# Kernel optimization log

Measured on AMD Instinct MI355X. Metric: run time of the kernel, lower is better.

Reference implementation:

```python
import jax, jax.numpy as jnp
import numpy as np

B, C, E, H = 8, 2048, 1024, 128


def setup_inputs() -> dict:
    key = jax.random.key(0)
    kx, kq, kk, kv = jax.random.split(key, 4)
    scale = 1.0 / np.sqrt(E)
    return {
        "x": jax.random.normal(kx, (B, C, E), dtype=jnp.float32),
        "Wq": jax.random.normal(kq, (E, H), dtype=jnp.float32) * scale,
        "Wk": jax.random.normal(kk, (E, H), dtype=jnp.float32) * scale,
        "Wv": jax.random.normal(kv, (E, H), dtype=jnp.float32) * scale,
    }


def reference(x, Wq, Wk, Wv):
    # x: (B, C, E); projections -> (B, C, H)
    q = jnp.einsum("bce,eh->bch", x, Wq)
    k = jnp.einsum("bce,eh->bch", x, Wk)
    v = jnp.einsum("bce,eh->bch", x, Wv)
    # NOTE: original scales by sqrt(embed_size), not head_size
    scores = jnp.einsum("bqh,bkh->bqk", q, k) / jnp.sqrt(jnp.asarray(E, x.dtype))
    Cq = x.shape[1]
    causal = jnp.tril(jnp.ones((Cq, Cq), dtype=bool))
    scores = jnp.where(causal, scores, -jnp.inf)
    weights = jax.nn.softmax(scores, axis=-1)  # (B, C, C)
    out = jnp.einsum("bqk,bkh->bqh", weights, v)
    return out
```

## Files before the change

kernel.cpp:

```cpp
#include <hip/hip_runtime.h>
#include <hip/hip_bf16.h>

#define BATCH 8
#define CTX   2048
#define EMB   1024
#define HD    128
#define VSTR  2080

using bf16x8 = __attribute__((ext_vector_type(8))) short;
using fx4    = __attribute__((ext_vector_type(4))) float;

__device__ __forceinline__ ushort f2bf(float f) {
    union { float f; unsigned u; } v; v.f = f;
    unsigned u = v.u;
    u += 0x7fffu + ((u >> 16) & 1u);
    return (ushort)(u >> 16);
}

__device__ __forceinline__ unsigned cvtpk(float a, float b) {
    unsigned r;
    asm("v_cvt_pk_bf16_f32 %0, %1, %2" : "=v"(r) : "v"(a), "v"(b));
    return r;
}

__device__ __forceinline__ void gload16(const void* g, void* l) {
    __builtin_amdgcn_global_load_lds(
        (const __attribute__((address_space(1))) unsigned*)g,
        (__attribute__((address_space(3))) unsigned*)l, 16, 0, 0);
}

__global__ void wt_kernel(const float* __restrict__ Wq, const float* __restrict__ Wk,
                          const float* __restrict__ Wv, ushort* __restrict__ Wt) {
    int idx = blockIdx.x * blockDim.x + threadIdx.x;
    int e = idx % EMB;
    int h = (idx / EMB) % HD;
    int w = idx / (EMB * HD);
    const float* W = (w == 0) ? Wq : (w == 1) ? Wk : Wv;
    Wt[idx] = f2bf(W[e * HD + h]);
}

__global__ __launch_bounds__(256) void proj_kernel(
        const float* __restrict__ x, const ushort* __restrict__ Wt,
        ushort* __restrict__ q, ushort* __restrict__ k, ushort* __restrict__ vt) {
    __shared__ __align__(16) char As[2][4096];
    __shared__ __align__(16) char Bs[2][24576];

    const int t    = threadIdx.x;
    const int wave = t >> 6;
    const int lane = t & 63;
    const int lo = lane & 15, hi = lane >> 4;
    const int brow = blockIdx.x * 32;

    fx4 acc[2][6];
#pragma unroll
    for (int m2 = 0; m2 < 2; m2++)
#pragma unroll
        for (int n = 0; n < 6; n++) acc[m2][n] = fx4{0.f, 0.f, 0.f, 0.f};

    const int arow  = t >> 3;
    const int aslot = (t & 7) ^ (arow & 7);
    const float* asrc = x + (size_t)(brow + arow) * EMB + aslot * 4;

    const ushort* bsrc[6];
#pragma unroll
    for (int r = 0; r < 6; r++) {
        const int lrow = r * 32 + (t >> 3);
        const int u    = (t & 7) ^ (lrow & 7);
        bsrc[r] = Wt + (size_t)(lrow * 2 + (u >> 2)) * EMB + (u & 3) * 8;
    }

#define PSTAGE(bi, k0_) do {                                          \
    gload16(asrc + (k0_), As[bi] + wave * 1024);                      \
    _Pragma("unroll")                                                 \
    for (int r = 0; r < 6; ++r)                                       \
        gload16(bsrc[r] + (k0_), Bs[bi] + r * 4096 + wave * 1024);    \
} while (0)

    PSTAGE(0, 0);
    for (int it = 0; it < 32; ++it) {
        if (it + 1 < 32) {
            PSTAGE((it + 1) & 1, (it + 1) * 32);
            asm volatile("s_waitcnt vmcnt(7)" ::: "memory");
        } else {
            asm volatile("s_waitcnt vmcnt(0)" ::: "memory");
        }
        __builtin_amdgcn_sched_barrier(0);
        __builtin_amdgcn_s_barrier();
        __builtin_amdgcn_sched_barrier(0);

        const char* Ab = As[it & 1];
        const char* Bb = Bs[it & 1];

        bf16x8 af[2];
#pragma unroll
        for (int m2 = 0; m2 < 2; m2++) {
            const int rowA = m2 * 16 + lo;
            const int s0 = (hi * 2) ^ (rowA & 7);
            const int s1 = (hi * 2 + 1) ^ (rowA & 7);
            fx4 a0 = *(const fx4*)(Ab + rowA * 128 + s0 * 16);
            fx4 a1 = *(const fx4*)(Ab + rowA * 128 + s1 * 16);
            union { unsigned u[4]; bf16x8 v; } pk;
            pk.u[0] = cvtpk(a0[0], a0[1]);
            pk.u[1] = cvtpk(a0[2], a0[3]);
            pk.u[2] = cvtpk(a1[0], a1[1]);
            pk.u[3] = cvtpk(a1[2], a1[3]);
            af[m2] = pk.v;
        }
        __builtin_amdgcn_s_setprio(1);
#pragma unroll
        for (int n = 0; n < 6; n++) {
            const int col  = wave * 96 + n * 16 + lo;
            const int rowp = col >> 1;
            const int slot = ((col & 1) * 4 + hi) ^ (rowp & 7);
            bf16x8 bfr = *(const bf16x8*)(Bb + rowp * 128 + slot * 16);
#pragma unroll
            for (int m2 = 0; m2 < 2; m2++)
                acc[m2][n] = __builtin_amdgcn_mfma_f32_16x16x32_bf16(af[m2], bfr, acc[m2][n], 0, 0, 0);
        }
        __builtin_amdgcn_s_setprio(0);
        __builtin_amdgcn_s_barrier();
    }
#undef PSTAGE

    const float qscale = 0.03125f;
#pragma unroll
    for (int n = 0; n < 6; n++) {
        const int col = wave * 96 + n * 16 + lo;
        const int bnn = col >> 7;
        const int cc  = col & 127;
#pragma unroll
        for (int m2 = 0; m2 < 2; m2++) {
#pragma unroll
            for (int j = 0; j < 4; j++) {
                const int r = brow + m2 * 16 + hi * 4 + j;
                if (bnn == 0)      q[(size_t)r * HD + cc] = f2bf(acc[m2][n][j] * qscale);
                else if (bnn == 1) k[(size_t)r * HD + cc] = f2bf(acc[m2][n][j]);
                else {
                    const int bb = r >> 11, ccc = r & (CTX - 1);
                    vt[((size_t)bb * HD + cc) * VSTR + ccc] = f2bf(acc[m2][n][j]);
                }
            }
        }
    }
}

__global__ __launch_bounds__(128) void attn_kernel(
        const ushort* __restrict__ q, const ushort* __restrict__ k,
        const ushort* __restrict__ vt, float* __restrict__ out) {
    __shared__ __align__(16) char Ks[2][16384];
    __shared__ __align__(16) char Vs[2][16384];
    __shared__ __align__(16) char p_lds[2][1024];

    const int id   = blockIdx.x;
    const int b    = id & 7;
    const int pos  = id >> 3;
    const int qt   = 127 - pos;
    const int q0   = qt * 16;
    const int t    = threadIdx.x;
    const int w    = t >> 6;
    const int lane = t & 63;
    const int lo = lane & 15, hi = lane >> 4;

    const ushort* qb = q  + (size_t)b * CTX * HD;
    const ushort* kb = k  + (size_t)b * CTX * HD;
    const ushort* vb = vt + (size_t)b * HD * VSTR;

    bf16x8 qf[4];
#pragma unroll
    for (int ks = 0; ks < 4; ks++)
        qf[ks] = *(const bf16x8*)(qb + (q0 + lo) * HD + ks * 32 + hi * 8);

    fx4 o[8];
#pragma unroll
    for (int h = 0; h < 8; h++) o[h] = fx4{0.f, 0.f, 0.f, 0.f};
    float m[4], l[4];
#pragma unroll
    for (int j = 0; j < 4; j++) { m[j] = 0.f; l[j] = 0.f; }

    const int krow = t >> 4;
    const int ksl  = ((t & 15) ^ (krow & 7)) << 3;
    const int vrow = t >> 3;
    const int vsl  = ((t & 7) ^ (vrow & 7)) << 3;

#define STAGE(bi, kv0_) do {                                          \
    _Pragma("unroll")                                                 \
    for (int r = 0; r < 8; ++r)                                       \
        gload16(kb + (size_t)((kv0_) + r * 8 + krow) * HD + ksl,      \
                Ks[bi] + r * 2048 + w * 1024);                        \
    _Pragma("unroll")                                                 \
    for (int r = 0; r < 8; ++r)                                       \
        gload16(vb + (size_t)(r * 16 + vrow) * VSTR + (kv0_) + vsl,   \
                Vs[bi] + r * 2048 + w * 1024);                        \
} while (0)

    const int nkv = qt / 4 + 1;
    STAGE(0, 0);
    for (int it = 0; it < nkv; ++it) {
        if (it + 1 < nkv) {
            STAGE((it + 1) & 1, (it + 1) * 64);
            asm volatile("s_waitcnt vmcnt(16)" ::: "memory");
        } else {
            asm volatile("s_waitcnt vmcnt(0)" ::: "memory");
        }
        __builtin_amdgcn_sched_barrier(0);
        __builtin_amdgcn_s_barrier();
        __builtin_amdgcn_sched_barrier(0);

        const char* Kb = Ks[it & 1];
        const char* Vb = Vs[it & 1];
        const int kv0 = it * 64;

        fx4 s[2];
        s[0] = fx4{0.f, 0.f, 0.f, 0.f};
        s[1] = fx4{0.f, 0.f, 0.f, 0.f};
        __builtin_amdgcn_s_setprio(1);
#pragma unroll
        for (int n2 = 0; n2 < 2; n2++) {
            const int row = w * 32 + n2 * 16 + lo;
            const unsigned sw = (unsigned)((row & 7) << 4);
#pragma unroll
            for (int ks = 0; ks < 4; ks++) {
                bf16x8 kf = *(const bf16x8*)(Kb + row * 256 + ((ks * 64 + hi * 16) ^ sw));
                s[n2] = __builtin_amdgcn_mfma_f32_16x16x32_bf16(qf[ks], kf, s[n2], 0, 0, 0);
            }
        }
        __builtin_amdgcn_s_setprio(0);

        const bool diag = (kv0 + 64 > q0);
        float pmax[4];
        int allok = 1;
#pragma unroll
        for (int j = 0; j < 4; j++) {
            const int r = q0 + hi * 4 + j;
            if (diag) {
#pragma unroll
                for (int n2 = 0; n2 < 2; n2++)
                    if ((kv0 + w * 32 + n2 * 16 + lo) > r) s[n2][j] = -INFINITY;
            }
            pmax[j] = fmaxf(s[0][j], s[1][j]);
            allok &= (pmax[j] <= m[j] + 16.0f);
        }
        if (!__all(allok)) {
#pragma unroll
            for (int j = 0; j < 4; j++) {
                float mx = pmax[j];
                mx = fmaxf(mx, __shfl_xor(mx, 1));
                mx = fmaxf(mx, __shfl_xor(mx, 2));
                mx = fmaxf(mx, __shfl_xor(mx, 4));
                mx = fmaxf(mx, __shfl_xor(mx, 8));
                const float mn = fmaxf(m[j], mx);
                const float f  = __expf(m[j] - mn);
                l[j] *= f;
#pragma unroll
                for (int h = 0; h < 8; h++) o[h][j] *= f;
                m[j] = mn;
            }
        }
#pragma unroll
        for (int j = 0; j < 4; j++) {
            float sum = 0.f;
#pragma unroll
            for (int n2 = 0; n2 < 2; n2++) {
                const float pv = __expf(s[n2][j] - m[j]);
                s[n2][j] = pv;
                sum += pv;
            }
            l[j] += sum;
            const int row = hi * 4 + j;
            const unsigned sw = (unsigned)((row & 3) << 4);
#pragma unroll
            for (int n2 = 0; n2 < 2; n2++) {
                const unsigned cb = (unsigned)((n2 * 16 + lo) * 2);
                *(ushort*)(p_lds[w] + row * 64 + (cb ^ sw)) = f2bf(s[n2][j]);
            }
        }
        asm volatile("" ::: "memory");
        bf16x8 pa = *(const bf16x8*)(p_lds[w] + lo * 64 + ((hi * 16) ^ ((lo & 3) << 4)));
        __builtin_amdgcn_s_setprio(1);
#pragma unroll
        for (int h = 0; h < 8; h++) {
            const int vr = h * 16 + lo;
            bf16x8 vf = *(const bf16x8*)(Vb + vr * 128 + ((w * 64 + hi * 16) ^ ((vr & 7) << 4)));
            o[h] = __builtin_amdgcn_mfma_f32_16x16x32_bf16(pa, vf, o[h], 0, 0, 0);
        }
        __builtin_amdgcn_s_setprio(0);
        __builtin_amdgcn_s_barrier();
    }
#undef STAGE

#pragma unroll
    for (int j = 0; j < 4; j++) {
        l[j] += __shfl_xor(l[j], 1);
        l[j] += __shfl_xor(l[j], 2);
        l[j] += __shfl_xor(l[j], 4);
        l[j] += __shfl_xor(l[j], 8);
    }

    float* oB  = (float*)Ks[0];
    float* mlB = (float*)Vs[0];
    __syncthreads();
    if (w == 1) {
#pragma unroll
        for (int j = 0; j < 4; j++) {
            const int row = hi * 4 + j;
            if (lo == 0) { mlB[row] = m[j]; mlB[16 + row] = l[j]; }
#pragma unroll
            for (int h = 0; h < 8; h++) oB[row * 128 + h * 16 + lo] = o[h][j];
        }
    }
    __syncthreads();
    if (w == 0) {
        float* ob = out + ((size_t)b * CTX + q0) * HD;
#pragma unroll
        for (int j = 0; j < 4; j++) {
            const int row = hi * 4 + j;
            const float mB = mlB[row], lB = mlB[16 + row];
            const float mt = fmaxf(m[j], mB);
            const float fA = __expf(m[j] - mt);
            const float fB = __expf(mB - mt);
            const float inv = 1.0f / (l[j] * fA + lB * fB);
#pragma unroll
            for (int h = 0; h < 8; h++)
                ob[row * HD + h * 16 + lo] =
                    (o[h][j] * fA + oB[row * 128 + h * 16 + lo] * fB) * inv;
        }
    }
}

extern "C" void kernel_launch(void* const* d_in, const int* in_sizes, int n_in,
                              void* d_out, int out_size, void* d_ws, size_t ws_size,
                              hipStream_t stream) {
    const float* x  = (const float*)d_in[0];
    const float* Wq = (const float*)d_in[1];
    const float* Wk = (const float*)d_in[2];
    const float* Wv = (const float*)d_in[3];

    ushort* Wt = (ushort*)d_ws;
    ushort* qw = (ushort*)((char*)d_ws + 786432);
    ushort* kw = qw + (size_t)BATCH * CTX * HD;
    ushort* vw = kw + (size_t)BATCH * CTX * HD;

    wt_kernel<<<(3 * HD * EMB) / 256, 256, 0, stream>>>(Wq, Wk, Wv, Wt);
    proj_kernel<<<(BATCH * CTX) / 32, 256, 0, stream>>>(x, Wt, qw, kw, vw);
    attn_kernel<<<1024, 128, 0, stream>>>(qw, kw, vw, (float*)d_out);
}
```

Measured before the change: 100.6 us.

## Share KV tiles across two query tiles per block and restructure projection pipeline

The attention kernel now runs 256 threads per block covering 32 query rows (two 16-row halves), so each staged K/V tile in LDS is reused by twice as many queries. The grid is halved and the causal tile order is reordered for load balance. The loop now issues the next stage after a full wait plus barrier, which removes the trailing barrier. The projection kernel triple-buffers the x tile and issues the next prefetch after the barrier, also dropping the trailing barrier. The trade-off is more LDS and registers per block and possibly less overlap between loads and compute in attention, since the wait is now vmcnt(0).

```diff
diff --git a/kernel.cpp b/kernel.cpp
--- a/kernel.cpp
+++ b/kernel.cpp
@@ -42,7 +42,7 @@
 __global__ __launch_bounds__(256) void proj_kernel(
         const float* __restrict__ x, const ushort* __restrict__ Wt,
         ushort* __restrict__ q, ushort* __restrict__ k, ushort* __restrict__ vt) {
-    __shared__ __align__(16) char As[2][4096];
+    __shared__ __align__(16) char As[3][4096];
     __shared__ __align__(16) char Bs[2][24576];
 
     const int t    = threadIdx.x;
@@ -69,26 +69,28 @@
         bsrc[r] = Wt + (size_t)(lrow * 2 + (u >> 2)) * EMB + (u & 3) * 8;
     }
 
-#define PSTAGE(bi, k0_) do {                                          \
-    gload16(asrc + (k0_), As[bi] + wave * 1024);                      \
-    _Pragma("unroll")                                                 \
-    for (int r = 0; r < 6; ++r)                                       \
-        gload16(bsrc[r] + (k0_), Bs[bi] + r * 4096 + wave * 1024);    \
-} while (0)
-
-    PSTAGE(0, 0);
+    gload16(asrc + 0, As[0] + wave * 1024);
+#pragma unroll
+    for (int r = 0; r < 6; ++r)
+        gload16(bsrc[r] + 0, Bs[0] + r * 4096 + wave * 1024);
+    gload16(asrc + 32, As[1] + wave * 1024);
+
     for (int it = 0; it < 32; ++it) {
-        if (it + 1 < 32) {
-            PSTAGE((it + 1) & 1, (it + 1) * 32);
-            asm volatile("s_waitcnt vmcnt(7)" ::: "memory");
-        } else {
-            asm volatile("s_waitcnt vmcnt(0)" ::: "memory");
-        }
+        if (it == 31) asm volatile("s_waitcnt vmcnt(0)" ::: "memory");
+        else          asm volatile("s_waitcnt vmcnt(1)" ::: "memory");
         __builtin_amdgcn_sched_barrier(0);
         __builtin_amdgcn_s_barrier();
         __builtin_amdgcn_sched_barrier(0);
 
-        const char* Ab = As[it & 1];
+        if (it + 1 < 32) {
+#pragma unroll
+            for (int r = 0; r < 6; ++r)
+                gload16(bsrc[r] + (it + 1) * 32, Bs[(it + 1) & 1] + r * 4096 + wave * 1024);
+            if (it + 2 < 32)
+                gload16(asrc + (it + 2) * 32, As[(it + 2) % 3] + wave * 1024);
+        }
+
+        const char* Ab = As[it % 3];
         const char* Bb = Bs[it & 1];
 
         bf16x8 af[2];
@@ -118,9 +120,7 @@
                 acc[m2][n] = __builtin_amdgcn_mfma_f32_16x16x32_bf16(af[m2], bfr, acc[m2][n], 0, 0, 0);
         }
         __builtin_amdgcn_s_setprio(0);
-        __builtin_amdgcn_s_barrier();
-    }
-#undef PSTAGE
+    }
 
     const float qscale = 0.03125f;
 #pragma unroll
@@ -144,22 +144,23 @@
     }
 }
 
-__global__ __launch_bounds__(128) void attn_kernel(
+__global__ __launch_bounds__(256) void attn_kernel(
         const ushort* __restrict__ q, const ushort* __restrict__ k,
         const ushort* __restrict__ vt, float* __restrict__ out) {
     __shared__ __align__(16) char Ks[2][16384];
     __shared__ __align__(16) char Vs[2][16384];
-    __shared__ __align__(16) char p_lds[2][1024];
+    __shared__ __align__(16) char p_lds[4][1024];
 
     const int id   = blockIdx.x;
     const int b    = id & 7;
     const int pos  = id >> 3;
-    const int qt   = 127 - pos;
-    const int q0   = qt * 16;
+    const int qt   = (pos < 32) ? (63 - pos) : (pos - 32);
     const int t    = threadIdx.x;
-    const int w    = t >> 6;
+    const int wave = t >> 6;
     const int lane = t & 63;
     const int lo = lane & 15, hi = lane >> 4;
+    const int wq = wave & 1, w = wave >> 1;
+    const int q0 = qt * 32 + wq * 16;
 
     const ushort* qb = q  + (size_t)b * CTX * HD;
     const ushort* kb = k  + (size_t)b * CTX * HD;
@@ -177,34 +178,29 @@
 #pragma unroll
     for (int j = 0; j < 4; j++) { m[j] = 0.f; l[j] = 0.f; }
 
-    const int krow = t >> 4;
-    const int ksl  = ((t & 15) ^ (krow & 7)) << 3;
-    const int vrow = t >> 3;
-    const int vsl  = ((t & 7) ^ (vrow & 7)) << 3;
-
-#define STAGE(bi, kv0_) do {                                          \
-    _Pragma("unroll")                                                 \
-    for (int r = 0; r < 8; ++r)                                       \
-        gload16(kb + (size_t)((kv0_) + r * 8 + krow) * HD + ksl,      \
-                Ks[bi] + r * 2048 + w * 1024);                        \
-    _Pragma("unroll")                                                 \
-    for (int r = 0; r < 8; ++r)                                       \
-        gload16(vb + (size_t)(r * 16 + vrow) * VSTR + (kv0_) + vsl,   \
-                Vs[bi] + r * 2048 + w * 1024);                        \
+#define STAGE(bi, kv0_) do {                                                   \
+    _Pragma("unroll")                                                          \
+    for (int r = 0; r < 4; ++r) {                                              \
+        const int row = r * 16 + (t >> 4);                                     \
+        gload16(kb + (size_t)((kv0_) + row) * HD + (((t & 15) ^ (row & 7)) << 3), \
+                Ks[bi] + r * 4096 + wave * 1024);                              \
+    }                                                                          \
+    _Pragma("unroll")                                                          \
+    for (int r = 0; r < 4; ++r) {                                              \
+        const int row = r * 32 + (t >> 3);                                     \
+        gload16(vb + (size_t)row * VSTR + (kv0_) + (((t & 7) ^ (row & 7)) << 3), \
+                Vs[bi] + r * 4096 + wave * 1024);                              \
+    }                                                                          \
 } while (0)
 
-    const int nkv = qt / 4 + 1;
+    const int nkv = qt / 2 + 1;
     STAGE(0, 0);
     for (int it = 0; it < nkv; ++it) {
-        if (it + 1 < nkv) {
-            STAGE((it + 1) & 1, (it + 1) * 64);
-            asm volatile("s_waitcnt vmcnt(16)" ::: "memory");
-        } else {
-            asm volatile("s_waitcnt vmcnt(0)" ::: "memory");
-        }
+        asm volatile("s_waitcnt vmcnt(0)" ::: "memory");
         __builtin_amdgcn_sched_barrier(0);
         __builtin_amdgcn_s_barrier();
         __builtin_amdgcn_sched_barrier(0);
+        if (it + 1 < nkv) STAGE((it + 1) & 1, (it + 1) * 64);
 
         const char* Kb = Ks[it & 1];
         const char* Vb = Vs[it & 1];
@@ -271,11 +267,11 @@
 #pragma unroll
             for (int n2 = 0; n2 < 2; n2++) {
                 const unsigned cb = (unsigned)((n2 * 16 + lo) * 2);
-                *(ushort*)(p_lds[w] + row * 64 + (cb ^ sw)) = f2bf(s[n2][j]);
+                *(ushort*)(p_lds[wave] + row * 64 + (cb ^ sw)) = f2bf(s[n2][j]);
             }
         }
         asm volatile("" ::: "memory");
-        bf16x8 pa = *(const bf16x8*)(p_lds[w] + lo * 64 + ((hi * 16) ^ ((lo & 3) << 4)));
+        bf16x8 pa = *(const bf16x8*)(p_lds[wave] + lo * 64 + ((hi * 16) ^ ((lo & 3) << 4)));
         __builtin_amdgcn_s_setprio(1);
 #pragma unroll
         for (int h = 0; h < 8; h++) {
@@ -284,7 +280,6 @@
             o[h] = __builtin_amdgcn_mfma_f32_16x16x32_bf16(pa, vf, o[h], 0, 0, 0);
         }
         __builtin_amdgcn_s_setprio(0);
-        __builtin_amdgcn_s_barrier();
     }
 #undef STAGE
 
@@ -303,9 +298,10 @@
 #pragma unroll
         for (int j = 0; j < 4; j++) {
             const int row = hi * 4 + j;
-            if (lo == 0) { mlB[row] = m[j]; mlB[16 + row] = l[j]; }
-#pragma unroll
-            for (int h = 0; h < 8; h++) oB[row * 128 + h * 16 + lo] = o[h][j];
+            if (lo == 0) { mlB[wq * 32 + row] = m[j]; mlB[wq * 32 + 16 + row] = l[j]; }
+#pragma unroll
+            for (int h = 0; h < 8; h++)
+                oB[(wq * 16 + row) * 128 + h * 16 + lo] = o[h][j];
         }
     }
     __syncthreads();
@@ -314,7 +310,7 @@
 #pragma unroll
         for (int j = 0; j < 4; j++) {
             const int row = hi * 4 + j;
-            const float mB = mlB[row], lB = mlB[16 + row];
+            const float mB = mlB[wq * 32 + row], lB = mlB[wq * 32 + 16 + row];
             const float mt = fmaxf(m[j], mB);
             const float fA = __expf(m[j] - mt);
             const float fB = __expf(mB - mt);
@@ -322,7 +318,7 @@
 #pragma unroll
             for (int h = 0; h < 8; h++)
                 ob[row * HD + h * 16 + lo] =
-                    (o[h][j] * fA + oB[row * 128 + h * 16 + lo] * fB) * inv;
+                    (o[h][j] * fA + oB[(wq * 16 + row) * 128 + h * 16 + lo] * fB) * inv;
         }
     }
 }
@@ -342,5 +338,5 @@
 
     wt_kernel<<<(3 * HD * EMB) / 256, 256, 0, stream>>>(Wq, Wk, Wv, Wt);
     proj_kernel<<<(BATCH * CTX) / 32, 256, 0, stream>>>(x, Wt, qw, kw, vw);
-    attn_kernel<<<1024, 128, 0, stream>>>(qw, kw, vw, (float*)d_out);
-}
+    attn_kernel<<<512, 256, 0, stream>>>(qw, kw, vw, (float*)d_out);
+}
```

After: 96.83 us. 3.7% less time.
